# Optimization experiments

Hardware: AMD Instinct MI355X
Metric: run time of the kernel (lower is better)

The kernel has to match this reference:

```python
import jax, jax.numpy as jnp
import numpy as np

B, L, D, H, K = 4, 2048, 256, 8, 32
DH = D // H
DE = 64          # d_edge
CLIP = 32        # relpos_clip


def _ln(x, g, b):
    mu = x.mean(-1, keepdims=True)
    var = ((x - mu) ** 2).mean(-1, keepdims=True)
    return (x - mu) / jnp.sqrt(var + 1e-5) * g + b


def _gelu(x):
    return jax.nn.gelu(x, approximate=False)  # torch nn.GELU default = exact erf


def _masked_softmax(logits, mask):
    logits = jnp.where(mask == 0, jnp.finfo(logits.dtype).min, logits)
    return jax.nn.softmax(logits, axis=-1)


def setup_inputs() -> dict:
    key = jax.random.key(0)
    ks = jax.random.split(key, 24)
    s = 0.02
    w = lambda i, shape: jax.random.normal(ks[i], shape, jnp.float32) * s
    p = {}
    p['x'] = jax.random.normal(ks[0], (B, L, D), jnp.float32)
    p['mask'] = jax.random.randint(ks[1], (B, L), 0, 2, jnp.int32)
    p['nbr_idx'] = jax.random.randint(ks[2], (B, L, K), 0, L, jnp.int32)
    p['nbr_mask'] = jax.random.randint(ks[3], (B, L, K), 0, 2, jnp.int32)
    p['rel_pos'] = jax.random.randint(ks[4], (B, L, K), 0, 2 * CLIP + 1, jnp.int32)
    p['g1'] = jnp.ones((D,)); p['b1'] = jnp.zeros((D,))
    p['wq'] = w(5, (D, D)); p['wk'] = w(6, (D, D)); p['wv'] = w(7, (D, D))
    p['relpos_emb'] = w(8, (2 * CLIP + 1, DE))
    p['we1'] = w(9, (DE, D)); p['be1'] = jnp.zeros((D,))
    p['we2'] = w(10, (D, 1)); p['be2'] = jnp.zeros((1,))
    p['wg1'] = w(11, (2 * D, D)); p['bg1'] = jnp.zeros((D,))
    p['wg2'] = w(12, (D, D)); p['bg2'] = jnp.zeros((D,))
    p['wlo'] = w(13, (D, D)); p['blo'] = jnp.zeros((D,))
    p['wqkv'] = w(14, (D, 3 * D)); p['wgo'] = w(15, (D, D))
    p['wf1'] = w(16, (D, D)); p['bf1'] = jnp.zeros((D,))
    p['wf2'] = w(17, (D, 2)); p['bf2'] = jnp.zeros((2,))
    p['g2'] = jnp.ones((D,)); p['b2'] = jnp.zeros((D,))
    p['wff1'] = w(18, (D, 4 * D)); p['bff1'] = jnp.zeros((4 * D,))
    p['wff2'] = w(19, (4 * D, D)); p['bff2'] = jnp.zeros((D,))
    return p


def _block(x, mask, nbr_idx, nbr_mask, rel_pos,
           g1, b1, wq, wk, wv, relpos_emb, we1, be1, we2, be2,
           wg1, bg1, wg2, bg2, wlo, blo, wqkv, wgo,
           wf1, bf1, wf2, bf2, g2, b2, wff1, bff1, wff2, bff2):
    mf = mask.astype(x.dtype)                       # [B,L]
    h = _ln(x, g1, b1)

    # ---- local graph attention (gather over K neighbors) ----
    neigh = jax.vmap(lambda hb, ib: hb[ib])(h, nbr_idx)     # [B,L,K,D]
    q = (h @ wq)[:, :, None, :]                             # [B,L,1,D]
    k = neigh @ wk                                          # [B,L,K,D]
    v = neigh @ wv
    attn = (q * k).sum(-1) / np.sqrt(D).astype(np.float32)  # [B,L,K]
    rel = jnp.clip(rel_pos, -CLIP, CLIP) + CLIP
    e = relpos_emb[rel]                                     # [B,L,K,DE]
    attn = attn + (_gelu(e @ we1 + be1) @ we2 + be2)[..., 0]
    amask = nbr_mask * mask[:, :, None]
    w = _masked_softmax(attn, amask)
    agg = jnp.einsum('blk,blkd->bld', w, v)
    agg = agg @ wlo + blo
    g = jax.nn.sigmoid(_gelu(jnp.concatenate([h, agg], -1) @ wg1 + bg1) @ wg2 + bg2)
    h_local = (h + g * agg) * mf[..., None]

    # ---- global linear attention ----
    qkv = h @ wqkv
    qg, kg, vg = jnp.split(qkv, 3, axis=-1)
    to_heads = lambda z: z.reshape(B, L, H, DH).transpose(0, 2, 1, 3)  # [B,H,L,DH]
    qg, kg, vg = to_heads(qg), to_heads(kg), to_heads(vg)
    phi = lambda z: jax.nn.elu(z) + 1.0
    qg, kg = phi(qg), phi(kg)
    m = mf[:, None, :, None]
    kg = kg * m
    vg = vg * m
    kv = jnp.einsum('bhld,bhlm->bhdm', kg, vg)
    z = 1.0 / (jnp.einsum('bhld,bhd->bhl', qg, kg.sum(axis=2)) + 1e-6)
    y = jnp.einsum('bhld,bhdm->bhlm', qg, kv) * z[..., None]
    y = y.transpose(0, 2, 1, 3).reshape(B, L, D)
    y = (y @ wgo) * mf[..., None]
    h_global = h + y

    # ---- gated fusion (softmax over 2 branches) ----
    fw = jax.nn.softmax(_gelu(h @ wf1 + bf1) @ wf2 + bf2, axis=-1)
    yc = fw[..., 0:1] * h_local + fw[..., 1:2] * h_global
    x2 = x + (yc - x)  # DropPath is identity in eval mode

    # ---- FFN ----
    hn = _ln(x2, g2, b2)
    ffn = _gelu(hn @ wff1 + bff1) @ wff2 + bff2
    out = (x2 + ffn) * mf[..., None]
    return out


def reference(x, mask, nbr_idx, nbr_mask, rel_pos,
              g1, b1, wq, wk, wv, relpos_emb, we1, be1, we2, be2,
              wg1, bg1, wg2, bg2, wlo, blo, wqkv, wgo,
              wf1, bf1, wf2, bf2, g2, b2, wff1, bff1, wff2, bff2):
    return _block(x, mask, nbr_idx, nbr_mask, rel_pos,
                  g1, b1, wq, wk, wv, relpos_emb, we1, be1, we2, be2,
                  wg1, bg1, wg2, bg2, wlo, blo, wqkv, wgo,
                  wf1, bf1, wf2, bf2, g2, b2, wff1, bff1, wff2, bff2)
```

## Files before the change

kernel.cpp:

```cpp
#include <hip/hip_runtime.h>
#include <math.h>

#define LSEQ 2048
#define BB 4
#define DD 256
#define NROWS (BB*LSEQ)

typedef unsigned short u16;
typedef unsigned int u32;
typedef short s16x8 __attribute__((ext_vector_type(8)));
typedef float f32x4 __attribute__((ext_vector_type(4)));

__device__ __forceinline__ float gelu_f(float x){
    return 0.5f*x*(1.0f+erff(x*0.70710678118654752440f));
}
__device__ __forceinline__ float phi_f(float z){ return z>0.f ? z+1.f : expf(z); }
__device__ __forceinline__ float bf2f(u16 u){ union{u32 i; float f;} x; x.i = ((u32)u)<<16; return x.f; }
__device__ __forceinline__ u16 f2bf(float f){ union{float f; u32 i;} x; x.f = f; u32 r = (x.i + 0x7fff + ((x.i>>16)&1)) >> 16; return (u16)r; }

struct TransDesc { const float* src; int dstoff; int K; int N; };
struct TransArgs { TransDesc d[11]; };

__global__ __launch_bounds__(256) void transpose_kernel(TransArgs args, u16* __restrict__ WT)
{
    TransDesc e = args.d[blockIdx.z];
    int kt = blockIdx.x, nt = blockIdx.y;
    if (kt*32 >= e.K || nt*32 >= e.N) return;
    __shared__ float tile[32][33];
    int tx = threadIdx.x & 31, ty = threadIdx.x >> 5;
    #pragma unroll
    for (int i=0;i<4;++i){
        int k = kt*32 + ty + i*8;
        tile[ty+i*8][tx] = e.src[(size_t)k*e.N + nt*32 + tx];
    }
    __syncthreads();
    #pragma unroll
    for (int i=0;i<4;++i){
        int n = nt*32 + ty + i*8;
        WT[e.dstoff + (size_t)n*e.K + kt*32 + tx] = f2bf(tile[tx][ty+i*8]);
    }
}

__global__ __launch_bounds__(256) void ln_kernel(
    const float* __restrict__ x, const float* __restrict__ g,
    const float* __restrict__ b, u16* __restrict__ out)
{
    int r = blockIdx.x; int t = threadIdx.x;
    size_t i = (size_t)r*DD + t;
    float v = x[i];
    float s = v, ss = v*v;
    #pragma unroll
    for (int o=32;o>=1;o>>=1){ s += __shfl_xor(s,o); ss += __shfl_xor(ss,o); }
    __shared__ float sh[8];
    int wave = t>>6, lane = t&63;
    if (lane==0){ sh[wave]=s; sh[4+wave]=ss; }
    __syncthreads();
    float S  = sh[0]+sh[1]+sh[2]+sh[3];
    float SS = sh[4]+sh[5]+sh[6]+sh[7];
    float mu  = S*(1.f/DD);
    float var = SS*(1.f/DD) - mu*mu;
    float inv = rsqrtf(var + 1e-5f);
    out[i] = f2bf((v-mu)*inv*g[t] + b[t]);
}

template<int ACT, bool FINAL, typename CT>
__global__ __launch_bounds__(256) void mgemm(
    const u16* __restrict__ A0, const u16* __restrict__ A1, int kswitch, int lda,
    const u16* __restrict__ WT, int Kd,
    const float* __restrict__ bias,
    CT* __restrict__ C, int ldc,
    const u16* __restrict__ addsrc, const int* __restrict__ rowmask)
{
    __shared__ u16 ldsA[2048];
    __shared__ u16 ldsB[4096];
    int t = threadIdx.x;
    int row0 = blockIdx.x*64, col0 = blockIdx.y*128;
    int l = t & 63, w = t >> 6;
    int wm = w >> 1, wn = w & 1;

    int ar = t >> 2, ao = t & 3;
    int aidx = (ar>>4)*512 + ao*128 + (ar&15)*8;
    int bc0 = t >> 2, bo = t & 3;
    int bidx0 = (bc0>>4)*512 + bo*128 + (bc0&15)*8;
    int bc1 = bc0 + 64;
    int bidx1 = (bc1>>4)*512 + bo*128 + (bc1&15)*8;

    f32x4 acc[2][4];
    #pragma unroll
    for (int mf=0;mf<2;++mf)
        #pragma unroll
        for (int nf=0;nf<4;++nf)
            acc[mf][nf] = (f32x4){0.f,0.f,0.f,0.f};

    for (int k0 = 0; k0 < Kd; k0 += 32){
        const u16* Ab = A0; int kk = k0;
        if (k0 >= kswitch){ Ab = A1; kk = k0 - kswitch; }
        uint4 av  = *(const uint4*)(Ab + (size_t)(row0+ar)*lda + kk + ao*8);
        uint4 bv0 = *(const uint4*)(WT + (size_t)(col0+bc0)*Kd + k0 + bo*8);
        uint4 bv1 = *(const uint4*)(WT + (size_t)(col0+bc1)*Kd + k0 + bo*8);
        __syncthreads();
        *(uint4*)&ldsA[aidx]  = av;
        *(uint4*)&ldsB[bidx0] = bv0;
        *(uint4*)&ldsB[bidx1] = bv1;
        __syncthreads();
        s16x8 af[2], bfr[4];
        #pragma unroll
        for (int mf=0;mf<2;++mf) af[mf] = *(s16x8*)&ldsA[(wm*2+mf)*512 + l*8];
        #pragma unroll
        for (int nf=0;nf<4;++nf) bfr[nf] = *(s16x8*)&ldsB[(wn*4+nf)*512 + l*8];
        #pragma unroll
        for (int mf=0; mf<2; ++mf)
            #pragma unroll
            for (int nf=0; nf<4; ++nf)
                acc[mf][nf] = __builtin_amdgcn_mfma_f32_16x16x32_bf16(af[mf], bfr[nf], acc[mf][nf], 0,0,0);
    }

    int lrow = (l>>4)*4, lcol = l&15;
    #pragma unroll
    for (int mf=0; mf<2; ++mf){
        #pragma unroll
        for (int nf=0; nf<4; ++nf){
            int col = col0 + wn*64 + nf*16 + lcol;
            float bv = bias ? bias[col] : 0.f;
            #pragma unroll
            for (int i=0;i<4;++i){
                int row = row0 + wm*32 + mf*16 + lrow + i;
                float v = acc[mf][nf][i] + bv;
                if (ACT==1) v = gelu_f(v);
                else if (ACT==2) v = 1.f/(1.f+expf(-v));
                if (FINAL){
                    float mfv = (float)rowmask[row];
                    v = (bf2f(addsrc[(size_t)row*ldc + col]) + v) * mfv;
                }
                if constexpr (sizeof(CT)==2) C[(size_t)row*ldc+col] = (CT)f2bf(v);
                else                         C[(size_t)row*ldc+col] = v;
            }
        }
    }
}

__global__ __launch_bounds__(256) void bias_tab_kernel(
    const float* __restrict__ emb, const float* __restrict__ we1,
    const float* __restrict__ be1, const float* __restrict__ we2,
    const float* __restrict__ be2, float* __restrict__ tab)
{
    int r = blockIdx.x; int j = threadIdx.x;
    float acc = be1[j];
    #pragma unroll 8
    for (int d=0; d<64; ++d) acc += emb[r*64+d]*we1[d*256+j];
    float tv = gelu_f(acc)*we2[j];
    #pragma unroll
    for (int o=32;o>=1;o>>=1) tv += __shfl_xor(tv,o);
    __shared__ float sh[4];
    int wave = j>>6, lane = j&63;
    if (lane==0) sh[wave]=tv;
    __syncthreads();
    if (j==0) tab[r] = sh[0]+sh[1]+sh[2]+sh[3] + be2[0];
}

__global__ __launch_bounds__(256) void nattn_kernel(
    const u16* __restrict__ nb,
    const int* __restrict__ nbr_idx, const int* __restrict__ nbr_mask,
    const int* __restrict__ rel_pos, const int* __restrict__ mask,
    const float* __restrict__ btab, u16* __restrict__ agg)
{
    int r = blockIdx.x;
    int b = r >> 11;
    int t = threadIdx.x, lane = t&63, wave = t>>6;
    __shared__ float s_w[32];
    __shared__ int   s_idx[32];
    __shared__ float s_agg[4][256];
    uint2 qu = *(const uint2*)&nb[(size_t)r*768 + lane*4];
    float q0 = bf2f(qu.x&0xffff), q1 = bf2f(qu.x>>16);
    float q2 = bf2f(qu.y&0xffff), q3 = bf2f(qu.y>>16);
    int mrow = mask[r];
    #pragma unroll
    for (int j=0;j<8;++j){
        int k = wave*8 + j;
        int idx = nbr_idx[r*32+k];
        size_t grow = ((size_t)(b<<11) + idx)*768;
        uint2 ku = *(const uint2*)&nb[grow + 256 + lane*4];
        float d = q0*bf2f(ku.x&0xffff) + q1*bf2f(ku.x>>16)
                + q2*bf2f(ku.y&0xffff) + q3*bf2f(ku.y>>16);
        #pragma unroll
        for (int o=32;o>=1;o>>=1) d += __shfl_xor(d,o);
        if (lane==0){
            int rp = rel_pos[r*32+k];
            rp = rp < -32 ? -32 : (rp > 32 ? 32 : rp);
            float logit = d*0.0625f + btab[rp+32];
            int am = nbr_mask[r*32+k] * mrow;
            s_w[k]  = am ? logit : -3.402823466e38f;
            s_idx[k] = idx;
        }
    }
    __syncthreads();
    if (wave==0){
        float lg = (lane<32) ? s_w[lane] : -3.402823466e38f;
        float m = lg;
        #pragma unroll
        for (int o=16;o>=1;o>>=1) m = fmaxf(m, __shfl_xor(m,o));
        float e = (lane<32) ? expf(lg-m) : 0.f;
        float ssum = e;
        #pragma unroll
        for (int o=16;o>=1;o>>=1) ssum += __shfl_xor(ssum,o);
        if (lane<32) s_w[lane] = e/ssum;
    }
    __syncthreads();
    float4 av = {0.f,0.f,0.f,0.f};
    #pragma unroll
    for (int j=0;j<8;++j){
        int k = wave*8 + j;
        float wk = s_w[k];
        size_t grow = ((size_t)(b<<11) + s_idx[k])*768;
        uint2 vu = *(const uint2*)&nb[grow + 512 + lane*4];
        av.x += wk*bf2f(vu.x&0xffff); av.y += wk*bf2f(vu.x>>16);
        av.z += wk*bf2f(vu.y&0xffff); av.w += wk*bf2f(vu.y>>16);
    }
    *(float4*)&s_agg[wave][lane*4] = av;
    __syncthreads();
    float sum = s_agg[0][t]+s_agg[1][t]+s_agg[2][t]+s_agg[3][t];
    agg[(size_t)r*256 + t] = f2bf(sum);
}

__global__ __launch_bounds__(256) void linstats_kernel(
    const u16* __restrict__ qkv, const int* __restrict__ mask,
    float* __restrict__ kv, float* __restrict__ ksum)
{
    int blk = blockIdx.x;
    int bh = blk >> 4, ch = blk & 15;
    int b = bh >> 3, hh = bh & 7;
    int t = threadIdx.x;
    int d = t >> 3, m4 = (t & 7)*4;
    __shared__ float sk[8][32], sv[8][32];
    float a0=0,a1=0,a2=0,a3=0, aks=0;
    int l0 = ch*128;
    int half = t >> 7, tt = t & 127;
    int lr = tt >> 4, e2 = (tt & 15)*2;
    for (int g8=0; g8<16; ++g8){
        int l = l0 + g8*8 + lr;
        size_t base = ((size_t)b*LSEQ + l)*768 + (half ? 512 : 256) + hh*32 + e2;
        u32 u = *(const u32*)&qkv[base];
        float mf = (float)mask[b*LSEQ + l];
        float x0 = bf2f((u16)(u & 0xffff));
        float x1 = bf2f((u16)(u >> 16));
        if (half==0){ sk[lr][e2] = phi_f(x0)*mf; sk[lr][e2+1] = phi_f(x1)*mf; }
        else        { sv[lr][e2] = x0*mf;        sv[lr][e2+1] = x1*mf; }
        __syncthreads();
        #pragma unroll
        for (int rr=0;rr<8;++rr){
            float kd = sk[rr][d];
            a0 += kd*sv[rr][m4]; a1 += kd*sv[rr][m4+1];
            a2 += kd*sv[rr][m4+2]; a3 += kd*sv[rr][m4+3];
            if ((t&7)==0) aks += kd;
        }
        __syncthreads();
    }
    size_t kb = (size_t)bh*1024 + d*32 + m4;
    atomicAdd(&kv[kb+0],a0); atomicAdd(&kv[kb+1],a1);
    atomicAdd(&kv[kb+2],a2); atomicAdd(&kv[kb+3],a3);
    if ((t&7)==0) atomicAdd(&ksum[bh*32+d], aks);
}

__global__ __launch_bounds__(256) void linapply_kernel(
    const u16* __restrict__ qkv, const float* __restrict__ kv,
    const float* __restrict__ ksum, u16* __restrict__ y)
{
    int r = blockIdx.x; int b = r >> 11;
    int t = threadIdx.x;
    __shared__ float sq[256];
    if (t < 128){
        u32 u = *(const u32*)&qkv[(size_t)r*768 + t*2];
        sq[t*2]   = phi_f(bf2f((u16)(u & 0xffff)));
        sq[t*2+1] = phi_f(bf2f((u16)(u >> 16)));
    }
    __syncthreads();
    int hh = t>>5, m = t&31;
    const float* kvb = &kv[(size_t)((b<<3)+hh)*1024 + m];
    const float* ksb = &ksum[((b<<3)+hh)*32];
    const float* sqh = &sq[hh*32];
    float acc=0.f, az=0.f;
    #pragma unroll
    for (int dd=0; dd<32; ++dd){
        float qd = sqh[dd];
        acc += qd * kvb[dd*32];
        az  += qd * ksb[dd];
    }
    y[(size_t)r*256 + t] = f2bf(acc / (az + 1e-6f));
}

__global__ __launch_bounds__(64) void fw_kernel(
    const u16* __restrict__ f1, const float* __restrict__ wf2,
    const float* __restrict__ bf2, float* __restrict__ fw)
{
    int r = blockIdx.x; int lane = threadIdx.x;
    uint2 fu = *(const uint2*)&f1[(size_t)r*256 + lane*4];
    float v0 = bf2f(fu.x&0xffff), v1 = bf2f(fu.x>>16);
    float v2 = bf2f(fu.y&0xffff), v3 = bf2f(fu.y>>16);
    int dd = lane*4;
    float p0 = v0*wf2[dd*2]   + v1*wf2[dd*2+2] + v2*wf2[dd*2+4] + v3*wf2[dd*2+6];
    float p1 = v0*wf2[dd*2+1] + v1*wf2[dd*2+3] + v2*wf2[dd*2+5] + v3*wf2[dd*2+7];
    #pragma unroll
    for (int o=32;o>=1;o>>=1){ p0 += __shfl_xor(p0,o); p1 += __shfl_xor(p1,o); }
    if (lane==0){
        float a0=p0+bf2[0], a1=p1+bf2[1];
        float mx = fmaxf(a0,a1);
        float e0=expf(a0-mx), e1=expf(a1-mx);
        float s = e0+e1;
        fw[r*2] = e0/s; fw[r*2+1] = e1/s;
    }
}

__global__ __launch_bounds__(128) void combine_kernel(
    const u16* __restrict__ h, const u16* __restrict__ agglo,
    const u16* __restrict__ g, const u16* __restrict__ ygo,
    const float* __restrict__ fw, const int* __restrict__ mask,
    const float* __restrict__ g2, const float* __restrict__ b2,
    u16* __restrict__ x2, u16* __restrict__ hn)
{
    int r = blockIdx.x, t = threadIdx.x;
    size_t i = (size_t)r*DD + t*2;
    float mf = (float)mask[r];
    u32 hu = *(const u32*)&h[i],  au = *(const u32*)&agglo[i];
    u32 gu = *(const u32*)&g[i],  yu = *(const u32*)&ygo[i];
    float f0 = fw[r*2], f1v = fw[r*2+1];
    float hv0 = bf2f((u16)(hu&0xffff)), hv1 = bf2f((u16)(hu>>16));
    float ag0 = bf2f((u16)(au&0xffff)), ag1 = bf2f((u16)(au>>16));
    float gg0 = bf2f((u16)(gu&0xffff)), gg1 = bf2f((u16)(gu>>16));
    float yy0 = bf2f((u16)(yu&0xffff)), yy1 = bf2f((u16)(yu>>16));
    float v0 = f0*((hv0 + gg0*ag0)*mf) + f1v*(hv0 + yy0*mf);
    float v1 = f0*((hv1 + gg1*ag1)*mf) + f1v*(hv1 + yy1*mf);
    *(u32*)&x2[i] = (u32)f2bf(v0) | ((u32)f2bf(v1)<<16);
    float s = v0+v1, ss = v0*v0+v1*v1;
    #pragma unroll
    for (int o=32;o>=1;o>>=1){ s += __shfl_xor(s,o); ss += __shfl_xor(ss,o); }
    __shared__ float sh[4];
    int wave = t>>6, lane = t&63;
    if (lane==0){ sh[wave]=s; sh[2+wave]=ss; }
    __syncthreads();
    float S  = sh[0]+sh[1];
    float SS = sh[2]+sh[3];
    float mu  = S*(1.f/DD);
    float var = SS*(1.f/DD) - mu*mu;
    float inv = rsqrtf(var + 1e-5f);
    int j0 = t*2;
    float o0 = (v0-mu)*inv*g2[j0]   + b2[j0];
    float o1 = (v1-mu)*inv*g2[j0+1] + b2[j0+1];
    *(u32*)&hn[i] = (u32)f2bf(o0) | ((u32)f2bf(o1)<<16);
}

extern "C" void kernel_launch(void* const* d_in, const int* in_sizes, int n_in,
                              void* d_out, int out_size, void* d_ws, size_t ws_size,
                              hipStream_t stream)
{
    const float* x        = (const float*)d_in[0];
    const int*   mask     = (const int*)  d_in[1];
    const int*   nbr_idx  = (const int*)  d_in[2];
    const int*   nbr_mask = (const int*)  d_in[3];
    const int*   rel_pos  = (const int*)  d_in[4];
    const float* g1   = (const float*)d_in[5];
    const float* b1   = (const float*)d_in[6];
    const float* wq   = (const float*)d_in[7];
    const float* wk   = (const float*)d_in[8];
    const float* wv   = (const float*)d_in[9];
    const float* relpos_emb = (const float*)d_in[10];
    const float* we1  = (const float*)d_in[11];
    const float* be1  = (const float*)d_in[12];
    const float* we2  = (const float*)d_in[13];
    const float* be2  = (const float*)d_in[14];
    const float* wg1  = (const float*)d_in[15];
    const float* bg1  = (const float*)d_in[16];
    const float* wg2  = (const float*)d_in[17];
    const float* bg2  = (const float*)d_in[18];
    const float* wlo  = (const float*)d_in[19];
    const float* blo  = (const float*)d_in[20];
    const float* wqkv = (const float*)d_in[21];
    const float* wgo  = (const float*)d_in[22];
    const float* wf1  = (const float*)d_in[23];
    const float* bf1  = (const float*)d_in[24];
    const float* wf2  = (const float*)d_in[25];
    const float* bf2  = (const float*)d_in[26];
    const float* g2   = (const float*)d_in[27];
    const float* b2   = (const float*)d_in[28];
    const float* wff1 = (const float*)d_in[29];
    const float* bff1 = (const float*)d_in[30];
    const float* wff2 = (const float*)d_in[31];
    const float* bff2 = (const float*)d_in[32];
    float* out = (float*)d_out;

    unsigned char* wsb = (unsigned char*)d_ws;
    u16* h_bf    = (u16*)(wsb + ((size_t)0<<20));
    u16* nb_bf   = (u16*)(wsb + ((size_t)4<<20));
    u16* agg_bf  = (u16*)(wsb + ((size_t)16<<20));
    u16* agglo_bf= (u16*)(wsb + ((size_t)20<<20));
    u16* t1_bf   = (u16*)(wsb + ((size_t)24<<20));
    u16* f1_bf   = (u16*)(wsb + ((size_t)28<<20));
    u16* ygo_bf  = (u16*)(wsb + ((size_t)32<<20));
    u16* ffn1_bf = (u16*)(wsb + ((size_t)36<<20));
    u16* WT      = (u16*)(wsb + ((size_t)52<<20));
    float* btab  = (float*)(wsb + ((size_t)56<<20));
    float* kvb   = btab + 128;
    float* ksb   = kvb + 32768;
    float* fwb   = ksb + 1024;

    const int WT_LOC  = 0;
    const int WT_LO   = 196608;
    const int WT_G1   = 262144;
    const int WT_G2   = 393216;
    const int WT_QKV  = 458752;
    const int WT_GO   = 655360;
    const int WT_F1   = 720896;
    const int WT_FF1  = 786432;
    const int WT_FF2  = 1048576;

    TransArgs ta;
    ta.d[0]  = { wq,              WT_LOC,           256, 256 };
    ta.d[1]  = { wk,              WT_LOC + 65536,   256, 256 };
    ta.d[2]  = { wv,              WT_LOC + 131072,  256, 256 };
    ta.d[3]  = { wlo,             WT_LO,            256, 256 };
    ta.d[4]  = { wg1,             WT_G1,            512, 256 };
    ta.d[5]  = { wg2,             WT_G2,            256, 256 };
    ta.d[6]  = { wqkv,            WT_QKV,           256, 768 };
    ta.d[7]  = { wgo,             WT_GO,            256, 256 };
    ta.d[8]  = { wf1,             WT_F1,            256, 256 };
    ta.d[9]  = { wff1,            WT_FF1,           256, 1024 };
    ta.d[10] = { wff2,            WT_FF2,           1024, 256 };

    const int KBIG = 1<<30;
    dim3 blk(256);

    transpose_kernel<<<dim3(32,32,11), blk, 0, stream>>>(ta, WT);
    ln_kernel<<<NROWS, blk, 0, stream>>>(x, g1, b1, h_bf);
    bias_tab_kernel<<<65, blk, 0, stream>>>(relpos_emb, we1, be1, we2, be2, btab);
    mgemm<0,false,u16><<<dim3(128,6), blk, 0, stream>>>(h_bf, h_bf, KBIG, 256, WT+WT_LOC, 256, nullptr, nb_bf, 768, nullptr, nullptr);
    nattn_kernel<<<NROWS, blk, 0, stream>>>(nb_bf, nbr_idx, nbr_mask, rel_pos, mask, btab, agg_bf);
    mgemm<0,false,u16><<<dim3(128,2), blk, 0, stream>>>(agg_bf, agg_bf, KBIG, 256, WT+WT_LO, 256, blo, agglo_bf, 256, nullptr, nullptr);
    mgemm<1,false,u16><<<dim3(128,2), blk, 0, stream>>>(h_bf, agglo_bf, 256, 256, WT+WT_G1, 512, bg1, t1_bf, 256, nullptr, nullptr);
    mgemm<2,false,u16><<<dim3(128,2), blk, 0, stream>>>(t1_bf, t1_bf, KBIG, 256, WT+WT_G2, 256, bg2, agg_bf, 256, nullptr, nullptr);
    mgemm<0,false,u16><<<dim3(128,6), blk, 0, stream>>>(h_bf, h_bf, KBIG, 256, WT+WT_QKV, 256, nullptr, nb_bf, 768, nullptr, nullptr);
    hipMemsetAsync(kvb, 0, (32768+1024)*sizeof(float), stream);
    linstats_kernel<<<512, blk, 0, stream>>>(nb_bf, mask, kvb, ksb);
    linapply_kernel<<<NROWS, blk, 0, stream>>>(nb_bf, kvb, ksb, t1_bf);
    mgemm<0,false,u16><<<dim3(128,2), blk, 0, stream>>>(t1_bf, t1_bf, KBIG, 256, WT+WT_GO, 256, nullptr, ygo_bf, 256, nullptr, nullptr);
    mgemm<1,false,u16><<<dim3(128,2), blk, 0, stream>>>(h_bf, h_bf, KBIG, 256, WT+WT_F1, 256, bf1, f1_bf, 256, nullptr, nullptr);
    fw_kernel<<<NROWS, dim3(64), 0, stream>>>(f1_bf, wf2, bf2, fwb);
    combine_kernel<<<NROWS, dim3(128), 0, stream>>>(h_bf, agglo_bf, agg_bf, ygo_bf, fwb, mask, g2, b2, t1_bf, f1_bf);
    mgemm<1,false,u16><<<dim3(128,8), blk, 0, stream>>>(f1_bf, f1_bf, KBIG, 256, WT+WT_FF1, 256, bff1, ffn1_bf, 1024, nullptr, nullptr);
    mgemm<0,true,float><<<dim3(128,2), blk, 0, stream>>>(ffn1_bf, ffn1_bf, KBIG, 1024, WT+WT_FF2, 1024, bff2, out, 256, t1_bf, mask);
}
```

Before: 345.7 us.

## Fuse all h-input projections into one wide GEMM and deepen GEMM K-tile

Merges the local QKV, global QKV and fusion-gate projections of the LN output into a single 1792-column GEMM. GELU is applied only to the trailing gate columns, so several small launches and repeated reads of h become one. The GEMM now stages 64-wide K tiles with register prefetch of the next tile, which halves the barrier count and overlaps global loads with MFMA work at the cost of more LDS. The neighbor-attention kernel issues all K and V gathers up front and uses a transposed butterfly reduction, and the transpose grid is flattened to skip empty blocks.

Result: faster. 296.6 us (-14.2%).

```diff
diff --git a/kernel.cpp b/kernel.cpp
--- a/kernel.cpp
+++ b/kernel.cpp
@@ -5,6 +5,7 @@
 #define BB 4
 #define DD 256
 #define NROWS (BB*LSEQ)
+#define LDBIG 1792
 
 typedef unsigned short u16;
 typedef unsigned int u32;
@@ -18,14 +19,19 @@
 __device__ __forceinline__ float bf2f(u16 u){ union{u32 i; float f;} x; x.i = ((u32)u)<<16; return x.f; }
 __device__ __forceinline__ u16 f2bf(float f){ union{float f; u32 i;} x; x.f = f; u32 r = (x.i + 0x7fff + ((x.i>>16)&1)) >> 16; return (u16)r; }
 
-struct TransDesc { const float* src; int dstoff; int K; int N; };
+struct TransDesc { const float* src; int dstoff; int K; int N; int tstart; };
 struct TransArgs { TransDesc d[11]; };
 
 __global__ __launch_bounds__(256) void transpose_kernel(TransArgs args, u16* __restrict__ WT)
 {
-    TransDesc e = args.d[blockIdx.z];
-    int kt = blockIdx.x, nt = blockIdx.y;
-    if (kt*32 >= e.K || nt*32 >= e.N) return;
+    int bid = blockIdx.x;
+    int z = 0;
+    #pragma unroll
+    for (int i=1;i<11;++i) if (bid >= args.d[i].tstart) z = i;
+    TransDesc e = args.d[z];
+    int tid = bid - e.tstart;
+    int ntx = e.N >> 5;
+    int kt = tid / ntx, nt = tid - kt*ntx;
     __shared__ float tile[32][33];
     int tx = threadIdx.x & 31, ty = threadIdx.x >> 5;
     #pragma unroll
@@ -39,6 +45,12 @@
         int n = nt*32 + ty + i*8;
         WT[e.dstoff + (size_t)n*e.K + kt*32 + tx] = f2bf(tile[tx][ty+i*8]);
     }
+}
+
+__global__ __launch_bounds__(256) void biasbig_kernel(const float* __restrict__ bf1, float* __restrict__ bb)
+{
+    int i = blockIdx.x*256 + threadIdx.x;
+    bb[i] = (i >= 1536) ? bf1[i-1536] : 0.f;
 }
 
 __global__ __launch_bounds__(256) void ln_kernel(
@@ -67,23 +79,22 @@
 __global__ __launch_bounds__(256) void mgemm(
     const u16* __restrict__ A0, const u16* __restrict__ A1, int kswitch, int lda,
     const u16* __restrict__ WT, int Kd,
-    const float* __restrict__ bias,
+    const float* __restrict__ bias, int actcol,
     CT* __restrict__ C, int ldc,
     const u16* __restrict__ addsrc, const int* __restrict__ rowmask)
 {
-    __shared__ u16 ldsA[2048];
-    __shared__ u16 ldsB[4096];
+    __shared__ u16 ldsA[4096];
+    __shared__ u16 ldsB[8192];
     int t = threadIdx.x;
     int row0 = blockIdx.x*64, col0 = blockIdx.y*128;
     int l = t & 63, w = t >> 6;
     int wm = w >> 1, wn = w & 1;
 
-    int ar = t >> 2, ao = t & 3;
-    int aidx = (ar>>4)*512 + ao*128 + (ar&15)*8;
-    int bc0 = t >> 2, bo = t & 3;
-    int bidx0 = (bc0>>4)*512 + bo*128 + (bc0&15)*8;
-    int bc1 = bc0 + 64;
-    int bidx1 = (bc1>>4)*512 + bo*128 + (bc1&15)*8;
+    int s_ar = t >> 2, s_ao = t & 3;
+    int aidx1 = (s_ar>>4)*1024 + s_ao*128 + (s_ar&15)*8;
+    int aidx2 = aidx1 + 4*128;
+    int s_bc = t >> 1, s_bo = (t & 1)*4;
+    int bbase = (s_bc>>4)*1024 + (s_bc&15)*8;
 
     f32x4 acc[2][4];
     #pragma unroll
@@ -92,27 +103,50 @@
         for (int nf=0;nf<4;++nf)
             acc[mf][nf] = (f32x4){0.f,0.f,0.f,0.f};
 
-    for (int k0 = 0; k0 < Kd; k0 += 32){
-        const u16* Ab = A0; int kk = k0;
-        if (k0 >= kswitch){ Ab = A1; kk = k0 - kswitch; }
-        uint4 av  = *(const uint4*)(Ab + (size_t)(row0+ar)*lda + kk + ao*8);
-        uint4 bv0 = *(const uint4*)(WT + (size_t)(col0+bc0)*Kd + k0 + bo*8);
-        uint4 bv1 = *(const uint4*)(WT + (size_t)(col0+bc1)*Kd + k0 + bo*8);
+    uint4 av1, av2, bv0, bv1, bv2, bv3;
+    {
+        const u16* Ab = A0; int kk = 0;
+        const u16* ap = Ab + (size_t)(row0+s_ar)*lda + kk;
+        av1 = *(const uint4*)(ap + s_ao*8);
+        av2 = *(const uint4*)(ap + 32 + s_ao*8);
+        const u16* bp = WT + (size_t)(col0 + s_bc)*Kd + s_bo*8;
+        bv0 = *(const uint4*)(bp); bv1 = *(const uint4*)(bp+8);
+        bv2 = *(const uint4*)(bp+16); bv3 = *(const uint4*)(bp+24);
+    }
+
+    for (int k0 = 0; k0 < Kd; k0 += 64){
         __syncthreads();
-        *(uint4*)&ldsA[aidx]  = av;
-        *(uint4*)&ldsB[bidx0] = bv0;
-        *(uint4*)&ldsB[bidx1] = bv1;
+        *(uint4*)&ldsA[aidx1] = av1;
+        *(uint4*)&ldsA[aidx2] = av2;
+        *(uint4*)&ldsB[bbase + (s_bo  )*128] = bv0;
+        *(uint4*)&ldsB[bbase + (s_bo+1)*128] = bv1;
+        *(uint4*)&ldsB[bbase + (s_bo+2)*128] = bv2;
+        *(uint4*)&ldsB[bbase + (s_bo+3)*128] = bv3;
         __syncthreads();
-        s16x8 af[2], bfr[4];
-        #pragma unroll
-        for (int mf=0;mf<2;++mf) af[mf] = *(s16x8*)&ldsA[(wm*2+mf)*512 + l*8];
-        #pragma unroll
-        for (int nf=0;nf<4;++nf) bfr[nf] = *(s16x8*)&ldsB[(wn*4+nf)*512 + l*8];
-        #pragma unroll
-        for (int mf=0; mf<2; ++mf)
+        int kn = k0 + 64;
+        if (kn < Kd){
+            const u16* Ab = A0; int kk = kn;
+            if (kn >= kswitch){ Ab = A1; kk = kn - kswitch; }
+            const u16* ap = Ab + (size_t)(row0+s_ar)*lda + kk;
+            av1 = *(const uint4*)(ap + s_ao*8);
+            av2 = *(const uint4*)(ap + 32 + s_ao*8);
+            const u16* bp = WT + (size_t)(col0 + s_bc)*Kd + kn + s_bo*8;
+            bv0 = *(const uint4*)(bp); bv1 = *(const uint4*)(bp+8);
+            bv2 = *(const uint4*)(bp+16); bv3 = *(const uint4*)(bp+24);
+        }
+        #pragma unroll
+        for (int s=0;s<2;++s){
+            s16x8 af[2], bfr[4];
             #pragma unroll
-            for (int nf=0; nf<4; ++nf)
-                acc[mf][nf] = __builtin_amdgcn_mfma_f32_16x16x32_bf16(af[mf], bfr[nf], acc[mf][nf], 0,0,0);
+            for (int mf=0;mf<2;++mf) af[mf] = *(s16x8*)&ldsA[(wm*2+mf)*1024 + (s*4+(l>>4))*128 + (l&15)*8];
+            #pragma unroll
+            for (int nf=0;nf<4;++nf) bfr[nf] = *(s16x8*)&ldsB[(wn*4+nf)*1024 + (s*4+(l>>4))*128 + (l&15)*8];
+            #pragma unroll
+            for (int mf=0; mf<2; ++mf)
+                #pragma unroll
+                for (int nf=0; nf<4; ++nf)
+                    acc[mf][nf] = __builtin_amdgcn_mfma_f32_16x16x32_bf16(af[mf], bfr[nf], acc[mf][nf], 0,0,0);
+        }
     }
 
     int lrow = (l>>4)*4, lcol = l&15;
@@ -126,7 +160,7 @@
             for (int i=0;i<4;++i){
                 int row = row0 + wm*32 + mf*16 + lrow + i;
                 float v = acc[mf][nf][i] + bv;
-                if (ACT==1) v = gelu_f(v);
+                if (ACT==1){ if (col >= actcol) v = gelu_f(v); }
                 else if (ACT==2) v = 1.f/(1.f+expf(-v));
                 if (FINAL){
                     float mfv = (float)rowmask[row];
@@ -168,30 +202,40 @@
     int b = r >> 11;
     int t = threadIdx.x, lane = t&63, wave = t>>6;
     __shared__ float s_w[32];
-    __shared__ int   s_idx[32];
     __shared__ float s_agg[4][256];
-    uint2 qu = *(const uint2*)&nb[(size_t)r*768 + lane*4];
+    uint2 qu = *(const uint2*)&nb[(size_t)r*LDBIG + lane*4];
     float q0 = bf2f(qu.x&0xffff), q1 = bf2f(qu.x>>16);
     float q2 = bf2f(qu.y&0xffff), q3 = bf2f(qu.y>>16);
     int mrow = mask[r];
+
+    uint2 kreg[8], vreg[8];
     #pragma unroll
     for (int j=0;j<8;++j){
-        int k = wave*8 + j;
-        int idx = nbr_idx[r*32+k];
-        size_t grow = ((size_t)(b<<11) + idx)*768;
-        uint2 ku = *(const uint2*)&nb[grow + 256 + lane*4];
-        float d = q0*bf2f(ku.x&0xffff) + q1*bf2f(ku.x>>16)
-                + q2*bf2f(ku.y&0xffff) + q3*bf2f(ku.y>>16);
-        #pragma unroll
-        for (int o=32;o>=1;o>>=1) d += __shfl_xor(d,o);
-        if (lane==0){
-            int rp = rel_pos[r*32+k];
-            rp = rp < -32 ? -32 : (rp > 32 ? 32 : rp);
-            float logit = d*0.0625f + btab[rp+32];
-            int am = nbr_mask[r*32+k] * mrow;
-            s_w[k]  = am ? logit : -3.402823466e38f;
-            s_idx[k] = idx;
-        }
+        int idx = nbr_idx[r*32 + wave*8 + j];
+        size_t grow = ((size_t)(b<<11) + idx)*LDBIG;
+        kreg[j] = *(const uint2*)&nb[grow + 256 + lane*4];
+        vreg[j] = *(const uint2*)&nb[grow + 512 + lane*4];
+    }
+    float d[8];
+    #pragma unroll
+    for (int j=0;j<8;++j){
+        d[j] = q0*bf2f(kreg[j].x&0xffff) + q1*bf2f(kreg[j].x>>16)
+             + q2*bf2f(kreg[j].y&0xffff) + q3*bf2f(kreg[j].y>>16);
+    }
+    #define CMB(a,b,s) ({ float _t = (lane&(s)) ? (a) : (b); float _r = __shfl_xor(_t,(s)); (lane&(s)) ? ((b)+_r) : ((a)+_r); })
+    float e10 = CMB(d[0],d[1],1), e11 = CMB(d[2],d[3],1);
+    float e12 = CMB(d[4],d[5],1), e13 = CMB(d[6],d[7],1);
+    float e20 = CMB(e10,e11,2),   e21 = CMB(e12,e13,2);
+    float e3  = CMB(e20,e21,4);
+    #undef CMB
+    e3 += __shfl_xor(e3,8); e3 += __shfl_xor(e3,16); e3 += __shfl_xor(e3,32);
+    if (lane < 8){
+        int k = wave*8 + lane;
+        int rp = rel_pos[r*32+k];
+        rp = rp < -32 ? -32 : (rp > 32 ? 32 : rp);
+        float logit = e3*0.0625f + btab[rp+32];
+        int am = nbr_mask[r*32+k] * mrow;
+        s_w[k] = am ? logit : -3.402823466e38f;
     }
     __syncthreads();
     if (wave==0){
@@ -209,12 +253,9 @@
     float4 av = {0.f,0.f,0.f,0.f};
     #pragma unroll
     for (int j=0;j<8;++j){
-        int k = wave*8 + j;
-        float wk = s_w[k];
-        size_t grow = ((size_t)(b<<11) + s_idx[k])*768;
-        uint2 vu = *(const uint2*)&nb[grow + 512 + lane*4];
-        av.x += wk*bf2f(vu.x&0xffff); av.y += wk*bf2f(vu.x>>16);
-        av.z += wk*bf2f(vu.y&0xffff); av.w += wk*bf2f(vu.y>>16);
+        float wk = s_w[wave*8 + j];
+        av.x += wk*bf2f(vreg[j].x&0xffff); av.y += wk*bf2f(vreg[j].x>>16);
+        av.z += wk*bf2f(vreg[j].y&0xffff); av.w += wk*bf2f(vreg[j].y>>16);
     }
     *(float4*)&s_agg[wave][lane*4] = av;
     __syncthreads();
@@ -238,7 +279,7 @@
     int lr = tt >> 4, e2 = (tt & 15)*2;
     for (int g8=0; g8<16; ++g8){
         int l = l0 + g8*8 + lr;
-        size_t base = ((size_t)b*LSEQ + l)*768 + (half ? 512 : 256) + hh*32 + e2;
+        size_t base = ((size_t)b*LSEQ + l)*LDBIG + (half ? 1280 : 1024) + hh*32 + e2;
         u32 u = *(const u32*)&qkv[base];
         float mf = (float)mask[b*LSEQ + l];
         float x0 = bf2f((u16)(u & 0xffff));
@@ -269,7 +310,7 @@
     int t = threadIdx.x;
     __shared__ float sq[256];
     if (t < 128){
-        u32 u = *(const u32*)&qkv[(size_t)r*768 + t*2];
+        u32 u = *(const u32*)&qkv[(size_t)r*LDBIG + 768 + t*2];
         sq[t*2]   = phi_f(bf2f((u16)(u & 0xffff)));
         sq[t*2+1] = phi_f(bf2f((u16)(u >> 16)));
     }
@@ -293,7 +334,7 @@
     const float* __restrict__ bf2, float* __restrict__ fw)
 {
     int r = blockIdx.x; int lane = threadIdx.x;
-    uint2 fu = *(const uint2*)&f1[(size_t)r*256 + lane*4];
+    uint2 fu = *(const uint2*)&f1[(size_t)r*LDBIG + 1536 + lane*4];
     float v0 = bf2f(fu.x&0xffff), v1 = bf2f(fu.x>>16);
     float v2 = bf2f(fu.y&0xffff), v3 = bf2f(fu.y>>16);
     int dd = lane*4;
@@ -388,62 +429,60 @@
     float* out = (float*)d_out;
 
     unsigned char* wsb = (unsigned char*)d_ws;
-    u16* h_bf    = (u16*)(wsb + ((size_t)0<<20));
-    u16* nb_bf   = (u16*)(wsb + ((size_t)4<<20));
-    u16* agg_bf  = (u16*)(wsb + ((size_t)16<<20));
-    u16* agglo_bf= (u16*)(wsb + ((size_t)20<<20));
-    u16* t1_bf   = (u16*)(wsb + ((size_t)24<<20));
-    u16* f1_bf   = (u16*)(wsb + ((size_t)28<<20));
-    u16* ygo_bf  = (u16*)(wsb + ((size_t)32<<20));
-    u16* ffn1_bf = (u16*)(wsb + ((size_t)36<<20));
-    u16* WT      = (u16*)(wsb + ((size_t)52<<20));
-    float* btab  = (float*)(wsb + ((size_t)56<<20));
-    float* kvb   = btab + 128;
+    u16* bigout  = (u16*)(wsb + ((size_t)0<<20));
+    u16* h_bf    = (u16*)(wsb + ((size_t)30<<20));
+    u16* agg_bf  = (u16*)(wsb + ((size_t)34<<20));
+    u16* agglo_bf= (u16*)(wsb + ((size_t)38<<20));
+    u16* x2y_bf  = (u16*)(wsb + ((size_t)42<<20));
+    u16* tg_bf   = (u16*)(wsb + ((size_t)46<<20));
+    u16* ygo_bf  = (u16*)(wsb + ((size_t)50<<20));
+    u16* hn_bf   = (u16*)(wsb + ((size_t)54<<20));
+    u16* WT      = (u16*)(wsb + ((size_t)58<<20));
+    float* btab  = (float*)(wsb + ((size_t)61<<20));
+    float* bbig  = btab + 128;
+    float* kvb   = bbig + 2048;
     float* ksb   = kvb + 32768;
     float* fwb   = ksb + 1024;
 
-    const int WT_LOC  = 0;
-    const int WT_LO   = 196608;
-    const int WT_G1   = 262144;
-    const int WT_G2   = 393216;
-    const int WT_QKV  = 458752;
-    const int WT_GO   = 655360;
-    const int WT_F1   = 720896;
+    const int WT_BIG  = 0;
+    const int WT_LO   = 458752;
+    const int WT_G1   = 524288;
+    const int WT_G2   = 655360;
+    const int WT_GO   = 720896;
     const int WT_FF1  = 786432;
     const int WT_FF2  = 1048576;
 
     TransArgs ta;
-    ta.d[0]  = { wq,              WT_LOC,           256, 256 };
-    ta.d[1]  = { wk,              WT_LOC + 65536,   256, 256 };
-    ta.d[2]  = { wv,              WT_LOC + 131072,  256, 256 };
-    ta.d[3]  = { wlo,             WT_LO,            256, 256 };
-    ta.d[4]  = { wg1,             WT_G1,            512, 256 };
-    ta.d[5]  = { wg2,             WT_G2,            256, 256 };
-    ta.d[6]  = { wqkv,            WT_QKV,           256, 768 };
-    ta.d[7]  = { wgo,             WT_GO,            256, 256 };
-    ta.d[8]  = { wf1,             WT_F1,            256, 256 };
-    ta.d[9]  = { wff1,            WT_FF1,           256, 1024 };
-    ta.d[10] = { wff2,            WT_FF2,           1024, 256 };
+    ta.d[0]  = { wq,   WT_BIG + 0,        256,  256,    0 };
+    ta.d[1]  = { wk,   WT_BIG + 65536,    256,  256,   64 };
+    ta.d[2]  = { wv,   WT_BIG + 131072,   256,  256,  128 };
+    ta.d[3]  = { wqkv, WT_BIG + 196608,   256,  768,  192 };
+    ta.d[4]  = { wf1,  WT_BIG + 393216,   256,  256,  384 };
+    ta.d[5]  = { wlo,  WT_LO,             256,  256,  448 };
+    ta.d[6]  = { wg1,  WT_G1,             512,  256,  512 };
+    ta.d[7]  = { wg2,  WT_G2,             256,  256,  640 };
+    ta.d[8]  = { wgo,  WT_GO,             256,  256,  704 };
+    ta.d[9]  = { wff1, WT_FF1,            256, 1024,  768 };
+    ta.d[10] = { wff2, WT_FF2,           1024,  256, 1024 };
 
     const int KBIG = 1<<30;
     dim3 blk(256);
 
-    transpose_kernel<<<dim3(32,32,11), blk, 0, stream>>>(ta, WT);
+    transpose_kernel<<<1280, blk, 0, stream>>>(ta, WT);
+    biasbig_kernel<<<7, blk, 0, stream>>>(bf1, bbig);
     ln_kernel<<<NROWS, blk, 0, stream>>>(x, g1, b1, h_bf);
     bias_tab_kernel<<<65, blk, 0, stream>>>(relpos_emb, we1, be1, we2, be2, btab);
-    mgemm<0,false,u16><<<dim3(128,6), blk, 0, stream>>>(h_bf, h_bf, KBIG, 256, WT+WT_LOC, 256, nullptr, nb_bf, 768, nullptr, nullptr);
-    nattn_kernel<<<NROWS, blk, 0, stream>>>(nb_bf, nbr_idx, nbr_mask, rel_pos, mask, btab, agg_bf);
-    mgemm<0,false,u16><<<dim3(128,2), blk, 0, stream>>>(agg_bf, agg_bf, KBIG, 256, WT+WT_LO, 256, blo, agglo_bf, 256, nullptr, nullptr);
-    mgemm<1,false,u16><<<dim3(128,2), blk, 0, stream>>>(h_bf, agglo_bf, 256, 256, WT+WT_G1, 512, bg1, t1_bf, 256, nullptr, nullptr);
-    mgemm<2,false,u16><<<dim3(128,2), blk, 0, stream>>>(t1_bf, t1_bf, KBIG, 256, WT+WT_G2, 256, bg2, agg_bf, 256, nullptr, nullptr);
-    mgemm<0,false,u16><<<dim3(128,6), blk, 0, stream>>>(h_bf, h_bf, KBIG, 256, WT+WT_QKV, 256, nullptr, nb_bf, 768, nullptr, nullptr);
     hipMemsetAsync(kvb, 0, (32768+1024)*sizeof(float), stream);
-    linstats_kernel<<<512, blk, 0, stream>>>(nb_bf, mask, kvb, ksb);
-    linapply_kernel<<<NROWS, blk, 0, stream>>>(nb_bf, kvb, ksb, t1_bf);
-    mgemm<0,false,u16><<<dim3(128,2), blk, 0, stream>>>(t1_bf, t1_bf, KBIG, 256, WT+WT_GO, 256, nullptr, ygo_bf, 256, nullptr, nullptr);
-    mgemm<1,false,u16><<<dim3(128,2), blk, 0, stream>>>(h_bf, h_bf, KBIG, 256, WT+WT_F1, 256, bf1, f1_bf, 256, nullptr, nullptr);
-    fw_kernel<<<NROWS, dim3(64), 0, stream>>>(f1_bf, wf2, bf2, fwb);
-    combine_kernel<<<NROWS, dim3(128), 0, stream>>>(h_bf, agglo_bf, agg_bf, ygo_bf, fwb, mask, g2, b2, t1_bf, f1_bf);
-    mgemm<1,false,u16><<<dim3(128,8), blk, 0, stream>>>(f1_bf, f1_bf, KBIG, 256, WT+WT_FF1, 256, bff1, ffn1_bf, 1024, nullptr, nullptr);
-    mgemm<0,true,float><<<dim3(128,2), blk, 0, stream>>>(ffn1_bf, ffn1_bf, KBIG, 1024, WT+WT_FF2, 1024, bff2, out, 256, t1_bf, mask);
-}
+    mgemm<1,false,u16><<<dim3(128,14), blk, 0, stream>>>(h_bf, h_bf, KBIG, 256, WT+WT_BIG, 256, bbig, 1536, bigout, LDBIG, nullptr, nullptr);
+    fw_kernel<<<NROWS, dim3(64), 0, stream>>>(bigout, wf2, bf2, fwb);
+    linstats_kernel<<<512, blk, 0, stream>>>(bigout, mask, kvb, ksb);
+    linapply_kernel<<<NROWS, blk, 0, stream>>>(bigout, kvb, ksb, x2y_bf);
+    mgemm<0,false,u16><<<dim3(128,2), blk, 0, stream>>>(x2y_bf, x2y_bf, KBIG, 256, WT+WT_GO, 256, nullptr, 0, ygo_bf, 256, nullptr, nullptr);
+    nattn_kernel<<<NROWS, blk, 0, stream>>>(bigout, nbr_idx, nbr_mask, rel_pos, mask, btab, agg_bf);
+    mgemm<0,false,u16><<<dim3(128,2), blk, 0, stream>>>(agg_bf, agg_bf, KBIG, 256, WT+WT_LO, 256, blo, 0, agglo_bf, 256, nullptr, nullptr);
+    mgemm<1,false,u16><<<dim3(128,2), blk, 0, stream>>>(h_bf, agglo_bf, 256, 256, WT+WT_G1, 512, bg1, 0, tg_bf, 256, nullptr, nullptr);
+    mgemm<2,false,u16><<<dim3(128,2), blk, 0, stream>>>(tg_bf, tg_bf, KBIG, 256, WT+WT_G2, 256, bg2, 0, agg_bf, 256, nullptr, nullptr);
+    combine_kernel<<<NROWS, dim3(128), 0, stream>>>(h_bf, agglo_bf, agg_bf, ygo_bf, fwb, mask, g2, b2, x2y_bf, hn_bf);
+    mgemm<1,false,u16><<<dim3(128,8), blk, 0, stream>>>(hn_bf, hn_bf, KBIG, 256, WT+WT_FF1, 256, bff1, 0, bigout, 1024, nullptr, nullptr);
+    mgemm<0,true,float><<<dim3(128,2), blk, 0, stream>>>(bigout, bigout, KBIG, 1024, WT+WT_FF2, 1024, bff2, 0, out, 256, x2y_bf, mask);
+}
```
